# Optimization experiments

Hardware: AMD Instinct MI355X
Metric: run time of the kernel (lower is better)

## Reference

```python
import jax, jax.numpy as jnp
import numpy as np

N_USERS = 100000
N_ITEMS = 200000
D = 64
N_LAYERS = 2
UI_EDGES = 3200000
SOC_EDGES = 1600000
EPS = 1e-5  # torch LayerNorm default


def setup_inputs() -> dict:
    key = jax.random.key(0)
    ks = jax.random.split(key, 10)
    user_emb = jax.random.normal(ks[0], (N_USERS, D), jnp.float32)
    item_emb = jax.random.normal(ks[1], (N_ITEMS, D), jnp.float32)
    ui_src = jax.random.randint(ks[2], (UI_EDGES,), 0, N_USERS, jnp.int32)
    ui_dst = jax.random.randint(ks[3], (UI_EDGES,), 0, N_ITEMS, jnp.int32)
    ui_val = jax.random.uniform(ks[4], (UI_EDGES,), jnp.float32)
    soc_src = jax.random.randint(ks[5], (SOC_EDGES,), 0, N_USERS, jnp.int32)
    soc_dst = jax.random.randint(ks[6], (SOC_EDGES,), 0, N_USERS, jnp.int32)
    soc_val = jax.random.uniform(ks[7], (SOC_EDGES,), jnp.float32)
    # learned params: shared ui_transform / social_transform Linear per layer, 2*n_layers LayerNorms
    W_ui = jax.random.normal(ks[8], (N_LAYERS, D, D), jnp.float32) / np.sqrt(D).astype(np.float32)
    b_ui = jnp.zeros((N_LAYERS, D), jnp.float32)
    W_soc = jax.random.normal(ks[9], (N_LAYERS, D, D), jnp.float32) / np.sqrt(D).astype(np.float32)
    b_soc = jnp.zeros((N_LAYERS, D), jnp.float32)
    ln_g = jnp.ones((2 * N_LAYERS, D), jnp.float32)
    ln_b = jnp.zeros((2 * N_LAYERS, D), jnp.float32)
    return dict(user_emb=user_emb, item_emb=item_emb, ui_src=ui_src, ui_dst=ui_dst,
                ui_val=ui_val, soc_src=soc_src, soc_dst=soc_dst, soc_val=soc_val,
                W_ui=W_ui, b_ui=b_ui, W_soc=W_soc, b_soc=b_soc, ln_g=ln_g, ln_b=ln_b)


def _layernorm(x, g, b):
    m = jnp.mean(x, axis=-1, keepdims=True)
    v = jnp.var(x, axis=-1, keepdims=True)  # biased, as torch LayerNorm
    return (x - m) * jax.lax.rsqrt(v + EPS) * g + b


def _spmm(src, dst, val, x, n_rows):
    # out[r] = sum_{e: src[e]==r} val[e] * x[dst[e]]  (COO SpMM)
    return jax.ops.segment_sum(val[:, None] * x[dst], src, num_segments=n_rows)


def reference(user_emb, item_emb, ui_src, ui_dst, ui_val, soc_src, soc_dst, soc_val,
              W_ui, b_ui, W_soc, b_soc, ln_g, ln_b):
    n_users = user_emb.shape[0]
    n_items = item_emb.shape[0]
    ui_list = [user_emb]
    soc_list = [user_emb]
    u, it, s = user_emb, item_emb, user_emb
    for i in range(N_LAYERS):
        # user-item bipartite propagation (item_user = transpose of user_item)
        agg_u = _spmm(ui_src, ui_dst, ui_val, it, n_users) @ W_ui[i] + b_ui[i]
        agg_i = _spmm(ui_dst, ui_src, ui_val, u, n_items) @ W_ui[i] + b_ui[i]
        u = _layernorm(u + agg_u, ln_g[2 * i], ln_b[2 * i])
        it = _layernorm(it + agg_i, ln_g[2 * i + 1], ln_b[2 * i + 1])
        ui_list.append(u)
        # social propagation (shares layer_norms[2i] params with user branch)
        agg_s = _spmm(soc_src, soc_dst, soc_val, s, n_users) @ W_soc[i] + b_soc[i]
        s = _layernorm(s + agg_s, ln_g[2 * i], ln_b[2 * i])
        soc_list.append(s)
    # dropout is identity in eval/reference mode
    return (jnp.stack(ui_list), jnp.stack(soc_list), it)
```

## Files before the change

### kernel.cpp

```cpp
#include <hip/hip_runtime.h>
#include <stdint.h>

static constexpr int NU    = 100000;
static constexpr int NI    = 200000;
static constexpr int D     = 64;
static constexpr int E_UI  = 3200000;
static constexpr int E_SOC = 1600000;
static constexpr int CH    = 8192;
static constexpr int BROWS = 512;
#define EPS_LN 1e-5f

typedef __attribute__((ext_vector_type(8))) short bf16x8;
typedef __attribute__((ext_vector_type(4))) float f32x4;

__device__ __forceinline__ unsigned short f2b(float f) {
    unsigned u = __float_as_uint(f);
    u = (u + 0x7FFFu + ((u >> 16) & 1u)) >> 16;
    return (unsigned short)u;
}
__device__ __forceinline__ float b2fs(unsigned short h) {
    return __uint_as_float((unsigned)h << 16);
}
__device__ __forceinline__ float b2f_lo(unsigned u) { return __uint_as_float(u << 16); }
__device__ __forceinline__ float b2f_hi(unsigned u) { return __uint_as_float(u & 0xFFFF0000u); }

__global__ void __launch_bounds__(256) bin_count(
    const int* __restrict__ rows, int E, int nblk, int nb, int* __restrict__ cnt)
{
    __shared__ int hist[512];
    int b = blockIdx.x, t = threadIdx.x;
    for (int i = t; i < nb; i += 256) hist[i] = 0;
    __syncthreads();
    int e0 = b * CH, e1 = min(E, e0 + CH);
    for (int e = e0 + t; e < e1; e += 256)
        atomicAdd(&hist[rows[e] >> 9], 1);
    __syncthreads();
    for (int i = t; i < nb; i += 256) cnt[i * nblk + b] = hist[i];
}

__global__ void scan_partial(const int* __restrict__ cnt, int* __restrict__ bsum, int n)
{
    __shared__ int lds[256];
    int i = blockIdx.x * 256 + threadIdx.x;
    lds[threadIdx.x] = (i < n) ? cnt[i] : 0;
    __syncthreads();
    for (int off = 128; off > 0; off >>= 1) {
        if (threadIdx.x < off) lds[threadIdx.x] += lds[threadIdx.x + off];
        __syncthreads();
    }
    if (threadIdx.x == 0) bsum[blockIdx.x] = lds[0];
}

__global__ void scan_bsums(int* __restrict__ bsum, int nb)
{
    __shared__ int lds[1024];
    int t = threadIdx.x;
    int v = (t < nb) ? bsum[t] : 0;
    lds[t] = v;
    __syncthreads();
    for (int off = 1; off < 1024; off <<= 1) {
        int add = (t >= off) ? lds[t - off] : 0;
        __syncthreads();
        lds[t] += add;
        __syncthreads();
    }
    if (t < nb) bsum[t] = lds[t] - v;
}

__global__ void scan_out(const int* __restrict__ cnt, const int* __restrict__ bsum,
                         int* __restrict__ ofs, int n)
{
    __shared__ int lds[256];
    int i = blockIdx.x * 256 + threadIdx.x;
    int v = (i < n) ? cnt[i] : 0;
    lds[threadIdx.x] = v;
    __syncthreads();
    for (int off = 1; off < 256; off <<= 1) {
        int add = (threadIdx.x >= off) ? lds[threadIdx.x - off] : 0;
        __syncthreads();
        lds[threadIdx.x] += add;
        __syncthreads();
    }
    if (i < n) ofs[i] = bsum[blockIdx.x] + lds[threadIdx.x] - v;
}

__global__ void __launch_bounds__(256) bin_scatter(
    const int* __restrict__ rows, const int* __restrict__ idxs, const float* __restrict__ vals,
    int E, int nblk, const int* __restrict__ ofs, int nb, int2* __restrict__ binned)
{
    __shared__ int cur[512];
    int b = blockIdx.x, t = threadIdx.x;
    for (int i = t; i < nb; i += 256) cur[i] = ofs[i * nblk + b];
    __syncthreads();
    int e0 = b * CH, e1 = min(E, e0 + CH);
    for (int e = e0 + t; e < e1; e += 256) {
        int row = rows[e];
        int bucket = row >> 9;
        int slot = atomicAdd(&cur[bucket], 1);
        unsigned pack = ((unsigned)(row & 511) << 23) | (unsigned)idxs[e];
        binned[slot] = make_int2((int)pack, __float_as_int(vals[e]));
    }
}

__global__ void __launch_bounds__(512) fine_scatter(
    const int2* __restrict__ binned, const int* __restrict__ ofs, int nblk, int nb,
    int E, int nrows, int* __restrict__ rowptr, int2* __restrict__ rec)
{
    __shared__ int hist[512];
    __shared__ int cur[512];
    int b = blockIdx.x, t = threadIdx.x;
    int beg = ofs[b * nblk];
    int end = (b + 1 < nb) ? ofs[(b + 1) * nblk] : E;

    hist[t] = 0;
    __syncthreads();
    for (int j = beg + t; j < end; j += 512)
        atomicAdd(&hist[((unsigned)binned[j].x) >> 23], 1);
    __syncthreads();
    int v = hist[t];
    for (int off = 1; off < 512; off <<= 1) {
        int add = (t >= off) ? hist[t - off] : 0;
        __syncthreads();
        hist[t] += add;
        __syncthreads();
    }
    int excl = hist[t] - v;
    cur[t] = excl;
    int grow = b * BROWS + t;
    if (grow <= nrows) rowptr[grow] = beg + excl;
    __syncthreads();
    for (int j = beg + t; j < end; j += 512) {
        int2 eb = binned[j];
        unsigned p = (unsigned)eb.x;
        int rl  = (int)(p >> 23);
        int idx = (int)(p & 0x7FFFFFu);
        int c = atomicAdd(&cur[rl], 1);
        rec[beg + c] = make_int2(idx, eb.y);
    }
}

__global__ void copy0_kernel(const float4* __restrict__ src, float4* __restrict__ a,
                             float4* __restrict__ b, int n4)
{
    int i = blockIdx.x * blockDim.x + threadIdx.x;
    if (i < n4) { float4 v = src[i]; a[i] = v; b[i] = v; }
}

struct TaskT {
    const float* x;
    unsigned short* tab;
    const float* W;
    int ntiles;
    int blk0;
    int nblk;
};

__device__ __forceinline__ void split_hi_lo(const f32x4 a, const f32x4 b,
                                            bf16x8& hi, bf16x8& lo)
{
    #pragma unroll
    for (int j = 0; j < 4; ++j) {
        unsigned short h = f2b(a[j]);
        hi[j] = (short)h;
        lo[j] = (short)f2b(a[j] - b2fs(h));
    }
    #pragma unroll
    for (int j = 0; j < 4; ++j) {
        unsigned short h = f2b(b[j]);
        hi[4 + j] = (short)h;
        lo[4 + j] = (short)f2b(b[j] - b2fs(h));
    }
}

__global__ void __launch_bounds__(256) btab3(TaskT t0, TaskT t1, TaskT t2)
{
    __shared__ float Wl[64 * 64];
    TaskT t = (blockIdx.x >= (unsigned)t2.blk0) ? t2
            : (blockIdx.x >= (unsigned)t1.blk0) ? t1 : t0;
    {
        const float4* W4 = (const float4*)t.W;
        float4* Wl4 = (float4*)Wl;
        for (int i = threadIdx.x; i < 1024; i += 256) Wl4[i] = W4[i];
    }
    __syncthreads();

    int wv   = threadIdx.x >> 6;
    int lane = threadIdx.x & 63;
    int g    = lane >> 4;
    int c    = lane & 15;

    bf16x8 Whi[2][4], Wlo[2][4];
    #pragma unroll
    for (int kt = 0; kt < 2; ++kt)
        #pragma unroll
        for (int nt = 0; nt < 4; ++nt)
            #pragma unroll
            for (int j = 0; j < 8; ++j) {
                float w = Wl[(kt * 32 + 8 * g + j) * 64 + nt * 16 + c];
                unsigned short h = f2b(w);
                Whi[kt][nt][j] = (short)h;
                Wlo[kt][nt][j] = (short)f2b(w - b2fs(h));
            }

    int stride = t.nblk * 4;
    for (int tile = (blockIdx.x - t.blk0) * 4 + wv; tile < t.ntiles; tile += stride) {
        int rowbase = tile * 16;
        const float* arow = t.x + (size_t)(rowbase + c) * 64 + 8 * g;
        f32x4 a00 = *(const f32x4*)(arow);
        f32x4 a01 = *(const f32x4*)(arow + 4);
        f32x4 a10 = *(const f32x4*)(arow + 32);
        f32x4 a11 = *(const f32x4*)(arow + 36);
        bf16x8 Ahi0, Alo0, Ahi1, Alo1;
        split_hi_lo(a00, a01, Ahi0, Alo0);
        split_hi_lo(a10, a11, Ahi1, Alo1);

        #pragma unroll
        for (int nt = 0; nt < 4; ++nt) {
            f32x4 z = {0.f, 0.f, 0.f, 0.f};
            z = __builtin_amdgcn_mfma_f32_16x16x32_bf16(Ahi0, Whi[0][nt], z, 0, 0, 0);
            z = __builtin_amdgcn_mfma_f32_16x16x32_bf16(Ahi1, Whi[1][nt], z, 0, 0, 0);
            z = __builtin_amdgcn_mfma_f32_16x16x32_bf16(Alo0, Whi[0][nt], z, 0, 0, 0);
            z = __builtin_amdgcn_mfma_f32_16x16x32_bf16(Alo1, Whi[1][nt], z, 0, 0, 0);
            z = __builtin_amdgcn_mfma_f32_16x16x32_bf16(Ahi0, Wlo[0][nt], z, 0, 0, 0);
            z = __builtin_amdgcn_mfma_f32_16x16x32_bf16(Ahi1, Wlo[1][nt], z, 0, 0, 0);
            #pragma unroll
            for (int reg = 0; reg < 4; ++reg)
                t.tab[(size_t)(rowbase + 4 * g + reg) * 64 + nt * 16 + c] = f2b(z[reg]);
        }
    }
}

struct TaskS {
    const unsigned short* gsrc;
    const float* xin;
    float* yout;
    const int* rowptr;
    const int2* recs;
    const float* bias;
    const float* gamma;
    const float* beta;
    int nrows;
    int blk0;
};

__global__ void __launch_bounds__(256) spmmln3(TaskS t0, TaskS t1, TaskS t2)
{
    TaskS t = (blockIdx.x >= (unsigned)t2.blk0) ? t2
            : (blockIdx.x >= (unsigned)t1.blk0) ? t1 : t0;
    int wid  = (blockIdx.x - t.blk0) * 4 + (threadIdx.x >> 6);
    int lane = threadIdx.x & 63;
    if (wid >= t.nrows) return;

    int g  = lane >> 3;
    int l8 = lane & 7;

    float a0[8], a1[8];
    #pragma unroll
    for (int m = 0; m < 8; ++m) { a0[m] = 0.f; a1[m] = 0.f; }

    int beg = t.rowptr[wid], end = t.rowptr[wid + 1];
    int j = beg + g;
    for (; j + 8 < end; j += 16) {
        int2 r0 = t.recs[j];
        int2 r1 = t.recs[j + 8];
        uint4 h0 = ((const uint4*)(t.gsrc + (size_t)r0.x * 64))[l8];
        uint4 h1 = ((const uint4*)(t.gsrc + (size_t)r1.x * 64))[l8];
        float w0 = __int_as_float(r0.y);
        float w1 = __int_as_float(r1.y);
        a0[0] += w0 * b2f_lo(h0.x); a0[1] += w0 * b2f_hi(h0.x);
        a0[2] += w0 * b2f_lo(h0.y); a0[3] += w0 * b2f_hi(h0.y);
        a0[4] += w0 * b2f_lo(h0.z); a0[5] += w0 * b2f_hi(h0.z);
        a0[6] += w0 * b2f_lo(h0.w); a0[7] += w0 * b2f_hi(h0.w);
        a1[0] += w1 * b2f_lo(h1.x); a1[1] += w1 * b2f_hi(h1.x);
        a1[2] += w1 * b2f_lo(h1.y); a1[3] += w1 * b2f_hi(h1.y);
        a1[4] += w1 * b2f_lo(h1.z); a1[5] += w1 * b2f_hi(h1.z);
        a1[6] += w1 * b2f_lo(h1.w); a1[7] += w1 * b2f_hi(h1.w);
    }
    for (; j < end; j += 8) {
        int2 r0 = t.recs[j];
        uint4 h0 = ((const uint4*)(t.gsrc + (size_t)r0.x * 64))[l8];
        float w0 = __int_as_float(r0.y);
        a0[0] += w0 * b2f_lo(h0.x); a0[1] += w0 * b2f_hi(h0.x);
        a0[2] += w0 * b2f_lo(h0.y); a0[3] += w0 * b2f_hi(h0.y);
        a0[4] += w0 * b2f_lo(h0.z); a0[5] += w0 * b2f_hi(h0.z);
        a0[6] += w0 * b2f_lo(h0.w); a0[7] += w0 * b2f_hi(h0.w);
    }
    float acc[8];
    #pragma unroll
    for (int m = 0; m < 8; ++m) acc[m] = a0[m] + a1[m];
    #pragma unroll
    for (int off = 8; off <= 32; off <<= 1)
        #pragma unroll
        for (int m = 0; m < 8; ++m)
            acc[m] += __shfl_xor(acc[m], off);

    const float4* xi = (const float4*)(t.xin + (size_t)wid * 64 + 8 * l8);
    const float4* bi = (const float4*)(t.bias + 8 * l8);
    float4 x0 = xi[0], x1 = xi[1];
    float4 bb0 = bi[0], bb1 = bi[1];
    float tv[8];
    tv[0] = x0.x + acc[0] + bb0.x; tv[1] = x0.y + acc[1] + bb0.y;
    tv[2] = x0.z + acc[2] + bb0.z; tv[3] = x0.w + acc[3] + bb0.w;
    tv[4] = x1.x + acc[4] + bb1.x; tv[5] = x1.y + acc[5] + bb1.y;
    tv[6] = x1.z + acc[6] + bb1.z; tv[7] = x1.w + acc[7] + bb1.w;

    float s = 0.f;
    #pragma unroll
    for (int m = 0; m < 8; ++m) s += tv[m];
    #pragma unroll
    for (int off = 1; off <= 4; off <<= 1) s += __shfl_xor(s, off);
    float mean = s * (1.0f / 64.0f);
    float q = 0.f;
    #pragma unroll
    for (int m = 0; m < 8; ++m) { float dv = tv[m] - mean; q += dv * dv; }
    #pragma unroll
    for (int off = 1; off <= 4; off <<= 1) q += __shfl_xor(q, off);
    float rs = rsqrtf(q * (1.0f / 64.0f) + EPS_LN);

    if (g == 0) {
        const float4* ga = (const float4*)(t.gamma + 8 * l8);
        const float4* be = (const float4*)(t.beta + 8 * l8);
        float4 g0 = ga[0], g1 = ga[1];
        float4 e0 = be[0], e1 = be[1];
        float4 y0, y1;
        y0.x = (tv[0] - mean) * rs * g0.x + e0.x;
        y0.y = (tv[1] - mean) * rs * g0.y + e0.y;
        y0.z = (tv[2] - mean) * rs * g0.z + e0.z;
        y0.w = (tv[3] - mean) * rs * g0.w + e0.w;
        y1.x = (tv[4] - mean) * rs * g1.x + e1.x;
        y1.y = (tv[5] - mean) * rs * g1.y + e1.y;
        y1.z = (tv[6] - mean) * rs * g1.z + e1.z;
        y1.w = (tv[7] - mean) * rs * g1.w + e1.w;
        float4* yo = (float4*)(t.yout + (size_t)wid * 64 + 8 * l8);
        yo[0] = y0;
        yo[1] = y1;
    }
}

extern "C" void kernel_launch(void* const* d_in, const int* in_sizes, int n_in,
                              void* d_out, int out_size, void* d_ws, size_t ws_size,
                              hipStream_t stream)
{
    const float* user_emb = (const float*)d_in[0];
    const float* item_emb = (const float*)d_in[1];
    const int*   ui_src   = (const int*)d_in[2];
    const int*   ui_dst   = (const int*)d_in[3];
    const float* ui_val   = (const float*)d_in[4];
    const int*   soc_src  = (const int*)d_in[5];
    const int*   soc_dst  = (const int*)d_in[6];
    const float* soc_val  = (const float*)d_in[7];
    const float* W_ui     = (const float*)d_in[8];
    const float* b_ui     = (const float*)d_in[9];
    const float* W_soc    = (const float*)d_in[10];
    const float* b_soc    = (const float*)d_in[11];
    const float* ln_g     = (const float*)d_in[12];
    const float* ln_b     = (const float*)d_in[13];

    float* out     = (float*)d_out;
    float* out_ui  = out;
    float* out_soc = out + (size_t)3 * NU * D;
    float* out_it  = out + (size_t)6 * NU * D;

    const int NBU = (NU + BROWS - 1) / BROWS;
    const int NBI = (NI + BROWS - 1) / BROWS;
    const int BLK_UI  = (E_UI  + CH - 1) / CH;
    const int BLK_SOC = (E_SOC + CH - 1) / CH;

    char* p = (char*)d_ws;
    auto take = [&](size_t bytes) { char* r = p; p += (bytes + 255) & ~(size_t)255; return r; };
    int2* rec_us = (int2*)take((size_t)E_UI * 8);
    int2* rec_ud = (int2*)take((size_t)E_UI * 8);
    int2* rec_ss = (int2*)take((size_t)E_SOC * 8);
    int2* binned = (int2*)take((size_t)E_UI * 8);
    int*  rp_us  = (int*)take((size_t)(NU + 1) * 4);
    int*  rp_ud  = (int*)take((size_t)(NI + 1) * 4);
    int*  rp_ss  = (int*)take((size_t)(NU + 1) * 4);
    int*  cnt    = (int*)take((size_t)NBI * BLK_UI * 4);
    int*  ofs    = (int*)take((size_t)NBI * BLK_UI * 4);
    int*  bsum   = (int*)take(1024 * 4);
    unsigned short* twi = (unsigned short*)take((size_t)NU * D * 2);
    unsigned short* tws = (unsigned short*)take((size_t)NU * D * 2);
    unsigned short* twu = (unsigned short*)binned;

    auto build_csr = [&](const int* rows, const int* idxs, const float* vals,
                         int E, int nblk, int nb, int nrows, int* rowptr, int2* rec) {
        bin_count<<<nblk, 256, 0, stream>>>(rows, E, nblk, nb, cnt);
        int n = nb * nblk;
        int sb = (n + 255) / 256;
        scan_partial<<<sb, 256, 0, stream>>>(cnt, bsum, n);
        scan_bsums<<<1, 1024, 0, stream>>>(bsum, sb);
        scan_out<<<sb, 256, 0, stream>>>(cnt, bsum, ofs, n);
        bin_scatter<<<nblk, 256, 0, stream>>>(rows, idxs, vals, E, nblk, ofs, nb, binned);
        fine_scatter<<<nb, 512, 0, stream>>>(binned, ofs, nblk, nb, E, nrows, rowptr, rec);
    };

    build_csr(ui_src,  ui_dst,  ui_val,  E_UI,  BLK_UI,  NBU, NU, rp_us, rec_us);
    build_csr(ui_dst,  ui_src,  ui_val,  E_UI,  BLK_UI,  NBI, NI, rp_ud, rec_ud);
    build_csr(soc_src, soc_dst, soc_val, E_SOC, BLK_SOC, NBU, NU, rp_ss, rec_ss);

    int n4 = NU * D / 4;
    copy0_kernel<<<(n4 + 255) / 256, 256, 0, stream>>>((const float4*)user_emb,
                                                       (float4*)out_ui, (float4*)out_soc, n4);

    const float* u0 = user_emb;
    float* u1 = out_ui + (size_t)NU * D;
    float* u2 = out_ui + (size_t)2 * NU * D;
    const float* s0 = user_emb;
    float* s1 = out_soc + (size_t)NU * D;
    float* s2 = out_soc + (size_t)2 * NU * D;

    int ublocks = (NU + 3) / 4;
    int iblocks = (NI + 3) / 4;
    int agrid   = iblocks + 2 * ublocks;

    const int TB_I = 1040, TB_U = 520, TB_S = 520;
    int tgrid = TB_I + TB_U + TB_S;
    const int TIL_I = NI / 16, TIL_U = NU / 16;

    {
        TaskT ta { item_emb, twu, W_ui + 0 * 4096, TIL_I, 0, TB_I };
        TaskT tb { u0,       twi, W_ui + 0 * 4096, TIL_U, TB_I, TB_U };
        TaskT tc { u0,       tws, W_soc + 0 * 4096, TIL_U, TB_I + TB_U, TB_S };
        btab3<<<tgrid, 256, 0, stream>>>(ta, tb, tc);
    }
    {
        TaskS si { twi, item_emb, out_it, rp_ud, rec_ud, b_ui + 0 * 64,
                   ln_g + 1 * 64, ln_b + 1 * 64, NI, 0 };
        TaskS su { twu, u0, u1, rp_us, rec_us, b_ui + 0 * 64,
                   ln_g + 0 * 64, ln_b + 0 * 64, NU, iblocks };
        TaskS ss { tws, s0, s1, rp_ss, rec_ss, b_soc + 0 * 64,
                   ln_g + 0 * 64, ln_b + 0 * 64, NU, iblocks + ublocks };
        spmmln3<<<agrid, 256, 0, stream>>>(si, su, ss);
    }

    {
        TaskT ta { out_it, twu, W_ui + 1 * 4096, TIL_I, 0, TB_I };
        TaskT tb { u1,     twi, W_ui + 1 * 4096, TIL_U, TB_I, TB_U };
        TaskT tc { s1,     tws, W_soc + 1 * 4096, TIL_U, TB_I + TB_U, TB_S };
        btab3<<<tgrid, 256, 0, stream>>>(ta, tb, tc);
    }
    {
        TaskS si { twi, out_it, out_it, rp_ud, rec_ud, b_ui + 1 * 64,
                   ln_g + 3 * 64, ln_b + 3 * 64, NI, 0 };
        TaskS su { twu, u1, u2, rp_us, rec_us, b_ui + 1 * 64,
                   ln_g + 2 * 64, ln_b + 2 * 64, NU, iblocks };
        TaskS ss { tws, s1, s2, rp_ss, rec_ss, b_soc + 1 * 64,
                   ln_g + 2 * 64, ln_b + 2 * 64, NU, iblocks + ublocks };
        spmmln3<<<agrid, 256, 0, stream>>>(si, su, ss);
    }
}
```

Measured before the change: 812.6 us.

## Batch three CSR builds into combined launches and deepen SpMM gather unroll

The three CSR constructions (user-item by src, by dst, social) now run as single batched kernels per stage, each block picking its task from its block index, with separate workspace buffers per graph. This cuts 18 small serialized launches to 6 and lets the smaller stages of the three graphs fill the GPU together. The SpMM inner loop now issues four independent row gathers per iteration instead of two, with a predicated tail, to keep more memory loads in flight. The cost is extra workspace for the duplicated binned, count and offset arrays, and higher register use in the SpMM kernel.

```diff
diff --git a/kernel.cpp b/kernel.cpp
--- a/kernel.cpp
+++ b/kernel.cpp
@@ -24,38 +24,55 @@
 __device__ __forceinline__ float b2f_lo(unsigned u) { return __uint_as_float(u << 16); }
 __device__ __forceinline__ float b2f_hi(unsigned u) { return __uint_as_float(u & 0xFFFF0000u); }
 
-__global__ void __launch_bounds__(256) bin_count(
-    const int* __restrict__ rows, int E, int nblk, int nb, int* __restrict__ cnt)
+__device__ __forceinline__ void fma8(float* a, float w, uint4 h) {
+    a[0] += w * b2f_lo(h.x); a[1] += w * b2f_hi(h.x);
+    a[2] += w * b2f_lo(h.y); a[3] += w * b2f_hi(h.y);
+    a[4] += w * b2f_lo(h.z); a[5] += w * b2f_hi(h.z);
+    a[6] += w * b2f_lo(h.w); a[7] += w * b2f_hi(h.w);
+}
+
+struct CntT { const int* rows; int E; int nblk; int nb; int* cnt; int blk0; };
+
+__global__ void __launch_bounds__(256) bin_count3(CntT c0, CntT c1, CntT c2)
 {
     __shared__ int hist[512];
-    int b = blockIdx.x, t = threadIdx.x;
-    for (int i = t; i < nb; i += 256) hist[i] = 0;
-    __syncthreads();
-    int e0 = b * CH, e1 = min(E, e0 + CH);
+    CntT c = (blockIdx.x >= (unsigned)c2.blk0) ? c2
+           : (blockIdx.x >= (unsigned)c1.blk0) ? c1 : c0;
+    int b = blockIdx.x - c.blk0, t = threadIdx.x;
+    for (int i = t; i < c.nb; i += 256) hist[i] = 0;
+    __syncthreads();
+    int e0 = b * CH, e1 = min(c.E, e0 + CH);
     for (int e = e0 + t; e < e1; e += 256)
-        atomicAdd(&hist[rows[e] >> 9], 1);
-    __syncthreads();
-    for (int i = t; i < nb; i += 256) cnt[i * nblk + b] = hist[i];
-}
-
-__global__ void scan_partial(const int* __restrict__ cnt, int* __restrict__ bsum, int n)
+        atomicAdd(&hist[c.rows[e] >> 9], 1);
+    __syncthreads();
+    for (int i = t; i < c.nb; i += 256) c.cnt[i * c.nblk + b] = hist[i];
+}
+
+struct ScanT { const int* cnt; int n; int* bsum; int* ofs; int blk0; };
+
+__global__ void scan_partial3(ScanT s0, ScanT s1, ScanT s2)
 {
     __shared__ int lds[256];
-    int i = blockIdx.x * 256 + threadIdx.x;
-    lds[threadIdx.x] = (i < n) ? cnt[i] : 0;
+    ScanT s = (blockIdx.x >= (unsigned)s2.blk0) ? s2
+            : (blockIdx.x >= (unsigned)s1.blk0) ? s1 : s0;
+    int bb = blockIdx.x - s.blk0;
+    int i = bb * 256 + threadIdx.x;
+    lds[threadIdx.x] = (i < s.n) ? s.cnt[i] : 0;
     __syncthreads();
     for (int off = 128; off > 0; off >>= 1) {
         if (threadIdx.x < off) lds[threadIdx.x] += lds[threadIdx.x + off];
         __syncthreads();
     }
-    if (threadIdx.x == 0) bsum[blockIdx.x] = lds[0];
-}
-
-__global__ void scan_bsums(int* __restrict__ bsum, int nb)
+    if (threadIdx.x == 0) s.bsum[bb] = lds[0];
+}
+
+__global__ void scan_bsums3(ScanT s0, ScanT s1, ScanT s2)
 {
     __shared__ int lds[1024];
+    ScanT s = (blockIdx.x == 2) ? s2 : (blockIdx.x == 1) ? s1 : s0;
+    int nb = (s.n + 255) / 256;
     int t = threadIdx.x;
-    int v = (t < nb) ? bsum[t] : 0;
+    int v = (t < nb) ? s.bsum[t] : 0;
     lds[t] = v;
     __syncthreads();
     for (int off = 1; off < 1024; off <<= 1) {
@@ -64,15 +81,17 @@
         lds[t] += add;
         __syncthreads();
     }
-    if (t < nb) bsum[t] = lds[t] - v;
-}
-
-__global__ void scan_out(const int* __restrict__ cnt, const int* __restrict__ bsum,
-                         int* __restrict__ ofs, int n)
+    if (t < nb) s.bsum[t] = lds[t] - v;
+}
+
+__global__ void scan_out3(ScanT s0, ScanT s1, ScanT s2)
 {
     __shared__ int lds[256];
-    int i = blockIdx.x * 256 + threadIdx.x;
-    int v = (i < n) ? cnt[i] : 0;
+    ScanT s = (blockIdx.x >= (unsigned)s2.blk0) ? s2
+            : (blockIdx.x >= (unsigned)s1.blk0) ? s1 : s0;
+    int bb = blockIdx.x - s.blk0;
+    int i = bb * 256 + threadIdx.x;
+    int v = (i < s.n) ? s.cnt[i] : 0;
     lds[threadIdx.x] = v;
     __syncthreads();
     for (int off = 1; off < 256; off <<= 1) {
@@ -81,41 +100,47 @@
         lds[threadIdx.x] += add;
         __syncthreads();
     }
-    if (i < n) ofs[i] = bsum[blockIdx.x] + lds[threadIdx.x] - v;
-}
-
-__global__ void __launch_bounds__(256) bin_scatter(
-    const int* __restrict__ rows, const int* __restrict__ idxs, const float* __restrict__ vals,
-    int E, int nblk, const int* __restrict__ ofs, int nb, int2* __restrict__ binned)
+    if (i < s.n) s.ofs[i] = s.bsum[bb] + lds[threadIdx.x] - v;
+}
+
+struct ScatT { const int* rows; const int* idxs; const float* vals;
+               int E; int nblk; const int* ofs; int nb; int2* binned; int blk0; };
+
+__global__ void __launch_bounds__(256) bin_scatter3(ScatT c0, ScatT c1, ScatT c2)
 {
     __shared__ int cur[512];
-    int b = blockIdx.x, t = threadIdx.x;
-    for (int i = t; i < nb; i += 256) cur[i] = ofs[i * nblk + b];
-    __syncthreads();
-    int e0 = b * CH, e1 = min(E, e0 + CH);
+    ScatT c = (blockIdx.x >= (unsigned)c2.blk0) ? c2
+            : (blockIdx.x >= (unsigned)c1.blk0) ? c1 : c0;
+    int b = blockIdx.x - c.blk0, t = threadIdx.x;
+    for (int i = t; i < c.nb; i += 256) cur[i] = c.ofs[i * c.nblk + b];
+    __syncthreads();
+    int e0 = b * CH, e1 = min(c.E, e0 + CH);
     for (int e = e0 + t; e < e1; e += 256) {
-        int row = rows[e];
+        int row = c.rows[e];
         int bucket = row >> 9;
         int slot = atomicAdd(&cur[bucket], 1);
-        unsigned pack = ((unsigned)(row & 511) << 23) | (unsigned)idxs[e];
-        binned[slot] = make_int2((int)pack, __float_as_int(vals[e]));
-    }
-}
-
-__global__ void __launch_bounds__(512) fine_scatter(
-    const int2* __restrict__ binned, const int* __restrict__ ofs, int nblk, int nb,
-    int E, int nrows, int* __restrict__ rowptr, int2* __restrict__ rec)
+        unsigned pack = ((unsigned)(row & 511) << 23) | (unsigned)c.idxs[e];
+        c.binned[slot] = make_int2((int)pack, __float_as_int(c.vals[e]));
+    }
+}
+
+struct FineT { const int2* binned; const int* ofs; int nblk; int nb;
+               int E; int nrows; int* rowptr; int2* rec; int blk0; };
+
+__global__ void __launch_bounds__(512) fine_scatter3(FineT c0, FineT c1, FineT c2)
 {
     __shared__ int hist[512];
     __shared__ int cur[512];
-    int b = blockIdx.x, t = threadIdx.x;
-    int beg = ofs[b * nblk];
-    int end = (b + 1 < nb) ? ofs[(b + 1) * nblk] : E;
+    FineT c = (blockIdx.x >= (unsigned)c2.blk0) ? c2
+            : (blockIdx.x >= (unsigned)c1.blk0) ? c1 : c0;
+    int b = blockIdx.x - c.blk0, t = threadIdx.x;
+    int beg = c.ofs[b * c.nblk];
+    int end = (b + 1 < c.nb) ? c.ofs[(b + 1) * c.nblk] : c.E;
 
     hist[t] = 0;
     __syncthreads();
     for (int j = beg + t; j < end; j += 512)
-        atomicAdd(&hist[((unsigned)binned[j].x) >> 23], 1);
+        atomicAdd(&hist[((unsigned)c.binned[j].x) >> 23], 1);
     __syncthreads();
     int v = hist[t];
     for (int off = 1; off < 512; off <<= 1) {
@@ -127,15 +152,15 @@
     int excl = hist[t] - v;
     cur[t] = excl;
     int grow = b * BROWS + t;
-    if (grow <= nrows) rowptr[grow] = beg + excl;
+    if (grow <= c.nrows) c.rowptr[grow] = beg + excl;
     __syncthreads();
     for (int j = beg + t; j < end; j += 512) {
-        int2 eb = binned[j];
+        int2 eb = c.binned[j];
         unsigned p = (unsigned)eb.x;
         int rl  = (int)(p >> 23);
         int idx = (int)(p & 0x7FFFFFu);
-        int c = atomicAdd(&cur[rl], 1);
-        rec[beg + c] = make_int2(idx, eb.y);
+        int cc = atomicAdd(&cur[rl], 1);
+        c.rec[beg + cc] = make_int2(idx, eb.y);
     }
 }
 
@@ -254,40 +279,47 @@
     int g  = lane >> 3;
     int l8 = lane & 7;
 
-    float a0[8], a1[8];
-    #pragma unroll
-    for (int m = 0; m < 8; ++m) { a0[m] = 0.f; a1[m] = 0.f; }
+    float accA[8], accB[8];
+    #pragma unroll
+    for (int m = 0; m < 8; ++m) { accA[m] = 0.f; accB[m] = 0.f; }
 
     int beg = t.rowptr[wid], end = t.rowptr[wid + 1];
-    int j = beg + g;
-    for (; j + 8 < end; j += 16) {
-        int2 r0 = t.recs[j];
-        int2 r1 = t.recs[j + 8];
+    int jb = beg;
+    for (; jb + 32 <= end; jb += 32) {
+        int2 r0 = t.recs[jb + g];
+        int2 r1 = t.recs[jb + 8 + g];
+        int2 r2 = t.recs[jb + 16 + g];
+        int2 r3 = t.recs[jb + 24 + g];
         uint4 h0 = ((const uint4*)(t.gsrc + (size_t)r0.x * 64))[l8];
         uint4 h1 = ((const uint4*)(t.gsrc + (size_t)r1.x * 64))[l8];
-        float w0 = __int_as_float(r0.y);
-        float w1 = __int_as_float(r1.y);
-        a0[0] += w0 * b2f_lo(h0.x); a0[1] += w0 * b2f_hi(h0.x);
-        a0[2] += w0 * b2f_lo(h0.y); a0[3] += w0 * b2f_hi(h0.y);
-        a0[4] += w0 * b2f_lo(h0.z); a0[5] += w0 * b2f_hi(h0.z);
-        a0[6] += w0 * b2f_lo(h0.w); a0[7] += w0 * b2f_hi(h0.w);
-        a1[0] += w1 * b2f_lo(h1.x); a1[1] += w1 * b2f_hi(h1.x);
-        a1[2] += w1 * b2f_lo(h1.y); a1[3] += w1 * b2f_hi(h1.y);
-        a1[4] += w1 * b2f_lo(h1.z); a1[5] += w1 * b2f_hi(h1.z);
-        a1[6] += w1 * b2f_lo(h1.w); a1[7] += w1 * b2f_hi(h1.w);
-    }
-    for (; j < end; j += 8) {
-        int2 r0 = t.recs[j];
+        uint4 h2 = ((const uint4*)(t.gsrc + (size_t)r2.x * 64))[l8];
+        uint4 h3 = ((const uint4*)(t.gsrc + (size_t)r3.x * 64))[l8];
+        fma8(accA, __int_as_float(r0.y), h0);
+        fma8(accB, __int_as_float(r1.y), h1);
+        fma8(accA, __int_as_float(r2.y), h2);
+        fma8(accB, __int_as_float(r3.y), h3);
+    }
+    int rem = end - jb;
+    if (rem > 0) {
+        int endm1 = end - 1;
+        int e0 = jb + g;
+        int2 r0 = t.recs[min(e0, endm1)];
+        float w0 = (e0 < end) ? __int_as_float(r0.y) : 0.f;
+        int2 r1, r2, r3;
+        float w1 = 0.f, w2 = 0.f, w3 = 0.f;
+        bool s1 = rem > 8, s2 = rem > 16, s3 = rem > 24;
+        if (s1) { int e = jb + 8 + g;  r1 = t.recs[min(e, endm1)]; w1 = (e < end) ? __int_as_float(r1.y) : 0.f; }
+        if (s2) { int e = jb + 16 + g; r2 = t.recs[min(e, endm1)]; w2 = (e < end) ? __int_as_float(r2.y) : 0.f; }
+        if (s3) { int e = jb + 24 + g; r3 = t.recs[min(e, endm1)]; w3 = (e < end) ? __int_as_float(r3.y) : 0.f; }
         uint4 h0 = ((const uint4*)(t.gsrc + (size_t)r0.x * 64))[l8];
-        float w0 = __int_as_float(r0.y);
-        a0[0] += w0 * b2f_lo(h0.x); a0[1] += w0 * b2f_hi(h0.x);
-        a0[2] += w0 * b2f_lo(h0.y); a0[3] += w0 * b2f_hi(h0.y);
-        a0[4] += w0 * b2f_lo(h0.z); a0[5] += w0 * b2f_hi(h0.z);
-        a0[6] += w0 * b2f_lo(h0.w); a0[7] += w0 * b2f_hi(h0.w);
+        if (s1) { uint4 h1 = ((const uint4*)(t.gsrc + (size_t)r1.x * 64))[l8]; fma8(accB, w1, h1); }
+        if (s2) { uint4 h2 = ((const uint4*)(t.gsrc + (size_t)r2.x * 64))[l8]; fma8(accA, w2, h2); }
+        if (s3) { uint4 h3 = ((const uint4*)(t.gsrc + (size_t)r3.x * 64))[l8]; fma8(accB, w3, h3); }
+        fma8(accA, w0, h0);
     }
     float acc[8];
     #pragma unroll
-    for (int m = 0; m < 8; ++m) acc[m] = a0[m] + a1[m];
+    for (int m = 0; m < 8; ++m) acc[m] = accA[m] + accB[m];
     #pragma unroll
     for (int off = 8; off <= 32; off <<= 1)
         #pragma unroll
@@ -366,37 +398,61 @@
     const int BLK_UI  = (E_UI  + CH - 1) / CH;
     const int BLK_SOC = (E_SOC + CH - 1) / CH;
 
+    const int N1 = NBU * BLK_UI;
+    const int N2 = NBI * BLK_UI;
+    const int N3 = NBU * BLK_SOC;
+    const int SB1 = (N1 + 255) / 256, SB2 = (N2 + 255) / 256, SB3 = (N3 + 255) / 256;
+
     char* p = (char*)d_ws;
     auto take = [&](size_t bytes) { char* r = p; p += (bytes + 255) & ~(size_t)255; return r; };
     int2* rec_us = (int2*)take((size_t)E_UI * 8);
     int2* rec_ud = (int2*)take((size_t)E_UI * 8);
     int2* rec_ss = (int2*)take((size_t)E_SOC * 8);
-    int2* binned = (int2*)take((size_t)E_UI * 8);
+    int2* bin1 = (int2*)take((size_t)E_UI * 8);
+    int2* bin2 = (int2*)take((size_t)E_UI * 8);
+    int2* bin3 = (int2*)take((size_t)E_SOC * 8);
     int*  rp_us  = (int*)take((size_t)(NU + 1) * 4);
     int*  rp_ud  = (int*)take((size_t)(NI + 1) * 4);
     int*  rp_ss  = (int*)take((size_t)(NU + 1) * 4);
-    int*  cnt    = (int*)take((size_t)NBI * BLK_UI * 4);
-    int*  ofs    = (int*)take((size_t)NBI * BLK_UI * 4);
-    int*  bsum   = (int*)take(1024 * 4);
+    int*  cnt1 = (int*)take((size_t)N1 * 4);
+    int*  cnt2 = (int*)take((size_t)N2 * 4);
+    int*  cnt3 = (int*)take((size_t)N3 * 4);
+    int*  ofs1 = (int*)take((size_t)N1 * 4);
+    int*  ofs2 = (int*)take((size_t)N2 * 4);
+    int*  ofs3 = (int*)take((size_t)N3 * 4);
+    int*  bs1 = (int*)take(1024 * 4);
+    int*  bs2 = (int*)take(1024 * 4);
+    int*  bs3 = (int*)take(1024 * 4);
     unsigned short* twi = (unsigned short*)take((size_t)NU * D * 2);
     unsigned short* tws = (unsigned short*)take((size_t)NU * D * 2);
-    unsigned short* twu = (unsigned short*)binned;
-
-    auto build_csr = [&](const int* rows, const int* idxs, const float* vals,
-                         int E, int nblk, int nb, int nrows, int* rowptr, int2* rec) {
-        bin_count<<<nblk, 256, 0, stream>>>(rows, E, nblk, nb, cnt);
-        int n = nb * nblk;
-        int sb = (n + 255) / 256;
-        scan_partial<<<sb, 256, 0, stream>>>(cnt, bsum, n);
-        scan_bsums<<<1, 1024, 0, stream>>>(bsum, sb);
-        scan_out<<<sb, 256, 0, stream>>>(cnt, bsum, ofs, n);
-        bin_scatter<<<nblk, 256, 0, stream>>>(rows, idxs, vals, E, nblk, ofs, nb, binned);
-        fine_scatter<<<nb, 512, 0, stream>>>(binned, ofs, nblk, nb, E, nrows, rowptr, rec);
-    };
-
-    build_csr(ui_src,  ui_dst,  ui_val,  E_UI,  BLK_UI,  NBU, NU, rp_us, rec_us);
-    build_csr(ui_dst,  ui_src,  ui_val,  E_UI,  BLK_UI,  NBI, NI, rp_ud, rec_ud);
-    build_csr(soc_src, soc_dst, soc_val, E_SOC, BLK_SOC, NBU, NU, rp_ss, rec_ss);
+    unsigned short* twu = (unsigned short*)bin1;
+
+    {
+        CntT c1 { ui_src,  E_UI,  BLK_UI,  NBU, cnt1, 0 };
+        CntT c2 { ui_dst,  E_UI,  BLK_UI,  NBI, cnt2, BLK_UI };
+        CntT c3 { soc_src, E_SOC, BLK_SOC, NBU, cnt3, 2 * BLK_UI };
+        bin_count3<<<2 * BLK_UI + BLK_SOC, 256, 0, stream>>>(c1, c2, c3);
+    }
+    {
+        ScanT s1 { cnt1, N1, bs1, ofs1, 0 };
+        ScanT s2 { cnt2, N2, bs2, ofs2, SB1 };
+        ScanT s3 { cnt3, N3, bs3, ofs3, SB1 + SB2 };
+        scan_partial3<<<SB1 + SB2 + SB3, 256, 0, stream>>>(s1, s2, s3);
+        scan_bsums3<<<3, 1024, 0, stream>>>(s1, s2, s3);
+        scan_out3<<<SB1 + SB2 + SB3, 256, 0, stream>>>(s1, s2, s3);
+    }
+    {
+        ScatT c1 { ui_src,  ui_dst,  ui_val,  E_UI,  BLK_UI,  ofs1, NBU, bin1, 0 };
+        ScatT c2 { ui_dst,  ui_src,  ui_val,  E_UI,  BLK_UI,  ofs2, NBI, bin2, BLK_UI };
+        ScatT c3 { soc_src, soc_dst, soc_val, E_SOC, BLK_SOC, ofs3, NBU, bin3, 2 * BLK_UI };
+        bin_scatter3<<<2 * BLK_UI + BLK_SOC, 256, 0, stream>>>(c1, c2, c3);
+    }
+    {
+        FineT f1 { bin1, ofs1, BLK_UI,  NBU, E_UI,  NU, rp_us, rec_us, 0 };
+        FineT f2 { bin2, ofs2, BLK_UI,  NBI, E_UI,  NI, rp_ud, rec_ud, NBU };
+        FineT f3 { bin3, ofs3, BLK_SOC, NBU, E_SOC, NU, rp_ss, rec_ss, NBU + NBI };
+        fine_scatter3<<<NBU + NBI + NBU, 512, 0, stream>>>(f1, f2, f3);
+    }
 
     int n4 = NU * D / 4;
     copy0_kernel<<<(n4 + 255) / 256, 256, 0, stream>>>((const float4*)user_emb,
```

After: 764.9 us. 1.06x faster.
